# Performance work log

Hardware: AMD Instinct MI355X
Metric: run time of the kernel (lower is better)

## Reference

```python
import jax, jax.numpy as jnp
import numpy as np

N = 20000      # nodes
E1 = 100000    # topo (2d) edges
E2 = 100000    # distance edges
HID = 128      # hidden_size
N2D = 128      # node_embed_size_2d
E2D = 64       # edge_embed_size_2d
EF = 128       # edge_feat_size
ET = 32        # edge_type_size
NRBF = 64
CUT = 6.0


def rbf_expand(d):
    # Gaussian radial basis with cosine cutoff envelope, d: [E]
    centers = jnp.linspace(0.0, CUT, NRBF)
    width = CUT / NRBF
    env = 0.5 * (jnp.cos(jnp.pi * jnp.clip(d / CUT, 0.0, 1.0)) + 1.0)
    return jnp.exp(-((d[:, None] - centers) ** 2) / (2.0 * width * width)) * env[:, None]


def setup_inputs() -> dict:
    key = jax.random.key(0)
    ks = jax.random.split(key, 20)
    s = 0.02
    return {
        "H": jax.random.normal(ks[0], (N, HID), jnp.float32),
        "V": jax.random.normal(ks[1], (N, HID, 3), jnp.float32),
        "Z": jax.random.normal(ks[2], (N, 3), jnp.float32) * 3.0,
        "layer_i": 0,
        "H_2d": jax.random.normal(ks[3], (N, N2D), jnp.float32),
        "mask_2d": jnp.ones((N,), bool),
        "E2d_idx": jax.random.randint(ks[4], (2, E1), 0, N),
        "E2d_feat": jax.random.normal(ks[5], (E2D, E1), jnp.float32),
        "Z_3d": jax.random.normal(ks[6], (N, 3), jnp.float32) * 3.0,
        "mask_3d": jnp.ones((N,), bool),
        "Edist_idx": jax.random.randint(ks[7], (2, E2), 0, N),
        "Edist_val": jax.random.uniform(ks[8], (E2,), jnp.float32) * CUT,
        "virtual_node_embed": jax.random.normal(ks[9], (1, N2D), jnp.float32),
        "edge_type_embed": jax.random.normal(ks[10], (3, ET), jnp.float32),
        "W_rbf": jax.random.normal(ks[11], (EF, NRBF), jnp.float32) * s,
        "W_e2d": jax.random.normal(ks[12], (EF, E2D), jnp.float32) * s,
        "W_i": jax.random.normal(ks[13], (HID, HID + N2D), jnp.float32) * s,
        "W_phi1": jax.random.normal(ks[14], (HID, HID + EF + ET), jnp.float32) * s,
        "b_phi1": jnp.zeros((HID,), jnp.float32),
        "W_phi2": jax.random.normal(ks[15], (3 * HID, HID), jnp.float32) * s,
        "b_phi2": jnp.zeros((3 * HID,), jnp.float32),
        "W_msg": jax.random.normal(ks[16], (3 * HID, NRBF), jnp.float32) * s,
        "b_msg": jnp.zeros((3 * HID,), jnp.float32),
    }


def reference(H, V, Z, layer_i, H_2d, mask_2d, E2d_idx, E2d_feat, Z_3d, mask_3d,
              Edist_idx, Edist_val, virtual_node_embed, edge_type_embed,
              W_rbf, W_e2d, W_i, W_phi1, b_phi1, W_phi2, b_phi2, W_msg, b_msg):
    n = H.shape[0]
    # mask_3d is all-True in this fixture => n_cond_3d == n (static shapes)
    nodes_real = jnp.concatenate([H, H_2d], axis=-1)                       # [n, h1+h2]
    virt = jnp.broadcast_to(virtual_node_embed, (n, virtual_node_embed.shape[1]))
    nodes_virt = jnp.concatenate([H, virt], axis=-1)                        # [n, h1+h2]
    nodes = jnp.concatenate([nodes_real, nodes_virt], axis=0) @ W_i.T      # [2n, h1]
    v = jnp.concatenate([V, jnp.zeros_like(V)], axis=0)                     # [2n, h1, 3]
    z = jnp.concatenate([Z, Z_3d], axis=0)                                  # [2n, 3]

    row_3d = jnp.arange(n)
    col_3d = jnp.arange(n) + n
    E3d = jnp.stack([jnp.concatenate([row_3d, col_3d]),
                     jnp.concatenate([col_3d, row_3d])], axis=0)            # [2, 2n]
    edges = jnp.concatenate([E2d_idx, E3d, Edist_idx], axis=-1)             # [2, E]
    e1, e3, e2 = E2d_idx.shape[1], E3d.shape[1], Edist_idx.shape[1]
    edge_type = jnp.concatenate([jnp.zeros((e1,), jnp.int32),
                                 jnp.ones((e3,), jnp.int32),
                                 jnp.full((e2,), 2, jnp.int32)])
    et = edge_type_embed[edge_type]                                         # [E, ET]
    attr2d = E2d_feat.T @ W_e2d.T                                           # [e1, EF]
    attr3d = jnp.zeros((e3, W_e2d.shape[0]), jnp.float32)                   # [e3, EF]
    attrd = rbf_expand(Edist_val) @ W_rbf.T                                 # [e2, EF]
    edge_attr = jnp.concatenate(
        [jnp.concatenate([attr2d, attr3d, attrd], axis=0), et], axis=-1)    # [E, EF+ET]

    # AdapterLayer: PaiNN-style equivariant message passing
    row, col = edges[0], edges[1]
    rel = z[row] - z[col]                                                   # [E, 3]
    dist = jnp.sqrt(jnp.sum(rel * rel, axis=-1) + 1e-8)                     # [E]
    unit = rel / dist[:, None]
    phi_in = jnp.concatenate([nodes[col], edge_attr], axis=-1)
    phi = jax.nn.silu(phi_in @ W_phi1.T + b_phi1) @ W_phi2.T + b_phi2       # [E, 3h]
    wd = rbf_expand(dist) @ W_msg.T + b_msg                                 # [E, 3h]
    m = phi * wd
    h = nodes.shape[1]
    s_msg, v_gate, r_gate = m[:, :h], m[:, h:2 * h], m[:, 2 * h:]
    dv = v[col] * v_gate[:, :, None] + unit[:, None, :] * r_gate[:, :, None]  # [E, h, 3]
    nn2 = nodes.shape[0]
    H_add = jax.ops.segment_sum(s_msg, row, num_segments=nn2)[:n]
    V_add = jax.ops.segment_sum(dv, row, num_segments=nn2)[:n]

    # eval-mode clamp
    H_add = jnp.clip(H_add, -100.0, 100.0)
    V_add = jnp.clip(V_add, -100.0, 100.0)

    mask_dist = jnp.zeros((n,), bool).at[Edist_idx[0]].set(True).at[Edist_idx[1]].set(True)
    update_mask = mask_2d | mask_3d | mask_dist
    H_add = jnp.where(update_mask[:, None], H_add, 0.0)
    V_add = jnp.where(update_mask[:, None, None], V_add, 0.0)
    return H_add, V_add
```

## Files before the change

### kernel.cpp

```cpp
#include <hip/hip_runtime.h>
#include <hip/hip_bf16.h>

#define NN   20000
#define E1N  100000
#define E2N  100000
#define NEFF 220000
#define TILE 64
#define NBLK ((NEFF + TILE - 1) / TILE)
#define NPAD (NBLK * TILE)
#define RBF_STEP   0.09523809523809523f
#define RBF_INV2W2 56.88888888888889f

typedef short  bf16x8 __attribute__((ext_vector_type(8)));
typedef float  f32x4  __attribute__((ext_vector_type(4)));

__device__ __forceinline__ float4 ld4(const float* p) {
    return *reinterpret_cast<const float4*>(p);
}
__device__ __forceinline__ ushort f2bf(float x) {
    __hip_bfloat16 h = __float2bfloat16(x);
    return *reinterpret_cast<ushort*>(&h);
}
__device__ __forceinline__ float bf2f(ushort u) {
    return __uint_as_float(((unsigned)u) << 16);
}
__device__ __forceinline__ float env_of(float d) {
    float x = fminf(fmaxf(d * (1.0f / 6.0f), 0.0f), 1.0f);
    return 0.5f * (__cosf(3.14159265358979f * x) + 1.0f);
}
__device__ __forceinline__ float clip100(float x) {
    return fminf(fmaxf(x, -100.f), 100.f);
}

__device__ __forceinline__ int edge_row(int eid, const int* __restrict__ E2d_idx,
                                        const int* __restrict__ Edist_idx) {
    if (eid < E1N) return E2d_idx[eid];
    if (eid < E1N + NN) return eid - E1N;
    return Edist_idx[eid - E1N - NN];
}

__global__ __launch_bounds__(256) void hist_kernel(
    const int* __restrict__ E2d_idx, const int* __restrict__ Edist_idx,
    int* __restrict__ hist) {
    int g = blockIdx.x * 256 + threadIdx.x;
    if (g < NEFF) atomicAdd(&hist[edge_row(g, E2d_idx, Edist_idx)], 1);
}

__global__ __launch_bounds__(256) void scan_kernel(
    const int* __restrict__ hist, int* __restrict__ start, int* __restrict__ cursor) {
    __shared__ int wsum[4];
    const int t = threadIdx.x;
    const int base = t * 80;
    int s = 0;
    for (int j = 0; j < 80; ++j) {
        int idx = base + j;
        if (idx < NN) s += hist[idx];
    }
    const int lane = t & 63, w = t >> 6;
    int v = s;
    for (int off = 1; off < 64; off <<= 1) {
        int x = __shfl_up(v, off, 64);
        if (lane >= off) v += x;
    }
    if (lane == 63) wsum[w] = v;
    __syncthreads();
    int woff = 0;
    for (int i = 0; i < w; ++i) woff += wsum[i];
    int run = woff + v - s;
    for (int j = 0; j < 80; ++j) {
        int idx = base + j;
        if (idx < NN) {
            start[idx] = run;
            cursor[idx] = run;
            run += hist[idx];
        }
    }
    if (t == 255) start[NN] = run;
}

__global__ __launch_bounds__(256) void scatter_kernel(
    const int* __restrict__ E2d_idx, const int* __restrict__ Edist_idx,
    int* __restrict__ cursor, int* __restrict__ order) {
    int g = blockIdx.x * 256 + threadIdx.x;
    if (g < NEFF) {
        int r = edge_row(g, E2d_idx, Edist_idx);
        int pos = atomicAdd(&cursor[r], 1);
        order[pos] = g;
    }
}

__global__ __launch_bounds__(256) void meta_kernel(
    const int* __restrict__ order, const int* __restrict__ E2d_idx,
    const int* __restrict__ Edist_idx, const float* __restrict__ Edist_val,
    const float* __restrict__ Z, const float* __restrict__ Z3d,
    int4* __restrict__ metaI, float4* __restrict__ metaF,
    float4* __restrict__ metaU) {
    int g = blockIdx.x * 256 + threadIdx.x;
    if (g >= NPAD) return;
    int eid = (g < NEFF) ? order[g] : -1;
    int row, col, ty, e2 = 0; float dval = 0.f;
    if (eid < 0)             { ty = 1; row = -1; col = 0; }
    else if (eid < E1N)      { ty = 0; row = E2d_idx[eid]; col = E2d_idx[E1N + eid]; e2 = eid; }
    else if (eid < E1N + NN) { ty = 1; int jj = eid - E1N; row = jj; col = jj + NN; }
    else { ty = 2; int g2 = eid - E1N - NN;
           row = Edist_idx[g2]; col = Edist_idx[E2N + g2]; dval = Edist_val[g2]; }
    int rs = (row < 0) ? 0 : row;
    float prx = Z[rs * 3], pry = Z[rs * 3 + 1], prz = Z[rs * 3 + 2];
    float pcx, pcy, pcz;
    if (col < NN) { pcx = Z[col * 3]; pcy = Z[col * 3 + 1]; pcz = Z[col * 3 + 2]; }
    else { int c = col - NN; pcx = Z3d[c * 3]; pcy = Z3d[c * 3 + 1]; pcz = Z3d[c * 3 + 2]; }
    float dx = prx - pcx, dy = pry - pcy, dz = prz - pcz;
    float dist = sqrtf(dx * dx + dy * dy + dz * dz + 1e-8f);
    float inv = 1.0f / dist;
    int vcol = (col < NN) ? col : -1;
    metaI[g] = make_int4(col, row, ty, e2);
    metaF[g] = make_float4(dist, dval, env_of(dist), env_of(dval));
    metaU[g] = (row >= 0)
        ? make_float4(dx * inv, dy * inv, dz * inv, __int_as_float(vcol))
        : make_float4(0.f, 0.f, 0.f, __int_as_float(-1));
}

__global__ __launch_bounds__(256) void prep_kernel(
    const float* __restrict__ W_phi1, const float* __restrict__ b_phi1,
    const float* __restrict__ W_e2d, const float* __restrict__ W_rbf,
    const float* __restrict__ W_phi2, const float* __restrict__ W_msg,
    const float* __restrict__ et, const float* __restrict__ W_i,
    ushort* __restrict__ W1c, ushort* __restrict__ W2b,
    ushort* __restrict__ Wmb, float* __restrict__ b_type,
    ushort* __restrict__ Wib) {
    int g = blockIdx.x * 256 + threadIdx.x;
    if (g < 32768) {
        int n = g >> 8, k = g & 255;
        float v;
        if (k < 128) v = W_phi1[n * 288 + k];
        else {
            int kk = k - 128;
            const float* Wsel = (kk < 64) ? W_e2d : W_rbf;
            int j = kk & 63;
            float s = 0.f;
            for (int a = 0; a < 128; ++a) s += W_phi1[n * 288 + 128 + a] * Wsel[a * 64 + j];
            v = s;
        }
        W1c[n * 256 + k] = f2bf(v);
    } else if (g < 81920) {
        int q = g - 32768; W2b[q] = f2bf(W_phi2[q]);
    } else if (g < 106496) {
        int q = g - 81920; Wmb[q] = f2bf(W_msg[q]);
    } else if (g < 106880) {
        int q = g - 106496; int ty = q >> 7, n = q & 127;
        float s = b_phi1[n];
        for (int a = 0; a < 32; ++a) s += W_phi1[n * 288 + 256 + a] * et[ty * 32 + a];
        b_type[q] = s;
    } else if (g < 139648) {
        int q = g - 106880; Wib[q] = f2bf(W_i[q]);
    }
}

__global__ __launch_bounds__(256) void featT_kernel(
    const float* __restrict__ feat, ushort* __restrict__ featTb) {
    __shared__ float tile[64][65];
    const int t = threadIdx.x;
    const int cbase = blockIdx.x * 64;
    for (int i = t; i < 64 * 64; i += 256) {
        int k = i >> 6, e = i & 63;
        tile[k][e] = (cbase + e < E1N) ? feat[(size_t)k * E1N + cbase + e] : 0.f;
    }
    __syncthreads();
    for (int i = t; i < 64 * 64; i += 256) {
        int e = i >> 6, k = i & 63;
        if (cbase + e < E1N) featTb[(size_t)(cbase + e) * 64 + k] = f2bf(tile[k][e]);
    }
}

__global__ __launch_bounds__(256, 2) void nodes_mfma_kernel(
    const float* __restrict__ H, const float* __restrict__ H2d,
    const float* __restrict__ virt, const ushort* __restrict__ Wib,
    ushort* __restrict__ nodesb) {
    __shared__ ushort A[64][264];
    __shared__ ushort WB[128][132];

    const int t = threadIdx.x;
    const int gbase = blockIdx.x * 64;

    for (int i = t; i < 64 * 64; i += 256) {
        int e = i >> 6, q = i & 63;
        int row = gbase + e;
        float4 v;
        if (q < 32)          v = ld4(H + (size_t)((row < NN) ? row : row - NN) * 128 + q * 4);
        else if (row < NN)   v = ld4(H2d + (size_t)row * 128 + (q - 32) * 4);
        else                 v = ld4(virt + (q - 32) * 4);
        ushort tmp[4] = {f2bf(v.x), f2bf(v.y), f2bf(v.z), f2bf(v.w)};
        *reinterpret_cast<uint2*>(&A[e][q * 4]) = *reinterpret_cast<const uint2*>(tmp);
    }
    for (int i = t; i < 128 * 16; i += 256) {
        int n = i >> 4, q = i & 15;
        *reinterpret_cast<uint4*>(&WB[n][q * 8]) =
            *reinterpret_cast<const uint4*>(Wib + (size_t)n * 256 + q * 8);
    }
    __syncthreads();

    const int w  = t >> 6, lane = t & 63;
    const int mh = w >> 1, nh = w & 1;
    const int lr = lane >> 4, lc = lane & 15;
    const int ar0 = mh * 32 + lc;

    f32x4 acc[2][4];
#pragma unroll
    for (int mt = 0; mt < 2; ++mt)
#pragma unroll
        for (int nt = 0; nt < 4; ++nt) acc[mt][nt] = (f32x4){0.f, 0.f, 0.f, 0.f};
#pragma unroll
    for (int ks = 0; ks < 4; ++ks) {
        bf16x8 a0 = *reinterpret_cast<const bf16x8*>(&A[ar0][ks * 32 + lr * 8]);
        bf16x8 a1 = *reinterpret_cast<const bf16x8*>(&A[ar0 + 16][ks * 32 + lr * 8]);
#pragma unroll
        for (int nt = 0; nt < 4; ++nt) {
            int n = nh * 64 + nt * 16 + lc;
            bf16x8 b = *reinterpret_cast<const bf16x8*>(&WB[n][ks * 32 + lr * 8]);
            acc[0][nt] = __builtin_amdgcn_mfma_f32_16x16x32_bf16(a0, b, acc[0][nt], 0, 0, 0);
            acc[1][nt] = __builtin_amdgcn_mfma_f32_16x16x32_bf16(a1, b, acc[1][nt], 0, 0, 0);
        }
    }
    __syncthreads();
    for (int i = t; i < 128 * 16; i += 256) {
        int n = i >> 4, q = i & 15;
        *reinterpret_cast<uint4*>(&WB[n][q * 8]) =
            *reinterpret_cast<const uint4*>(Wib + (size_t)n * 256 + 128 + q * 8);
    }
    __syncthreads();
#pragma unroll
    for (int ks = 4; ks < 8; ++ks) {
        bf16x8 a0 = *reinterpret_cast<const bf16x8*>(&A[ar0][ks * 32 + lr * 8]);
        bf16x8 a1 = *reinterpret_cast<const bf16x8*>(&A[ar0 + 16][ks * 32 + lr * 8]);
#pragma unroll
        for (int nt = 0; nt < 4; ++nt) {
            int n = nh * 64 + nt * 16 + lc;
            bf16x8 b = *reinterpret_cast<const bf16x8*>(&WB[n][(ks - 4) * 32 + lr * 8]);
            acc[0][nt] = __builtin_amdgcn_mfma_f32_16x16x32_bf16(a0, b, acc[0][nt], 0, 0, 0);
            acc[1][nt] = __builtin_amdgcn_mfma_f32_16x16x32_bf16(a1, b, acc[1][nt], 0, 0, 0);
        }
    }
#pragma unroll
    for (int mt = 0; mt < 2; ++mt)
#pragma unroll
        for (int nt = 0; nt < 4; ++nt)
#pragma unroll
            for (int r = 0; r < 4; ++r) {
                int e  = mh * 32 + mt * 16 + lr * 4 + r;
                int ch = nh * 64 + nt * 16 + lc;
                nodesb[(size_t)(gbase + e) * 128 + ch] = f2bf(acc[mt][nt][r]);
            }
}

__global__ __launch_bounds__(256, 2) void edge1_kernel(
    const ushort* __restrict__ nodesb, const ushort* __restrict__ featTb,
    const ushort* __restrict__ W1c, const ushort* __restrict__ W2b,
    const ushort* __restrict__ Wmb, const float* __restrict__ b_type,
    const float* __restrict__ b_phi2, const float* __restrict__ b_msg,
    const int4* __restrict__ metaI, const float4* __restrict__ metaF,
    ushort* __restrict__ payloadM) {

    __shared__ ushort A1f[TILE * 264 + 256];
    __shared__ ushort WB[128][132];
    __shared__ float  s_bt[3][128];
    __shared__ int    s_col[TILE], s_ty[TILE], s_e2[TILE];
    __shared__ float  s_dval[TILE], s_env2[TILE];

    ushort* hidp  = A1f;
    ushort* m_lds = A1f + 8704;

    const int t = threadIdx.x;
    const int gbase = blockIdx.x * TILE;

    if (t < TILE) {
        int4 mi = metaI[gbase + t];
        s_col[t] = mi.x; s_ty[t] = mi.z; s_e2[t] = mi.w;
        float4 mf = metaF[gbase + t];
        s_dval[t] = mf.y; s_env2[t] = mf.w;
    }
    for (int i = t; i < 384; i += 256) ((float*)s_bt)[i] = b_type[i];
    __syncthreads();

    for (int i = t; i < TILE * 16; i += 256) {
        int e = i >> 4, q = i & 15;
        *reinterpret_cast<uint4*>(&A1f[e * 264 + q * 8]) =
            *reinterpret_cast<const uint4*>(nodesb + (size_t)s_col[e] * 128 + q * 8);
    }
    for (int i = t; i < TILE * 128; i += 256) {
        int e = i >> 7, k = i & 127;
        int ty = s_ty[e];
        ushort v = 0;
        if (ty == 0) { if (k < 64) v = featTb[(size_t)s_e2[e] * 64 + k]; }
        else if (ty == 2) {
            if (k >= 64) {
                float dd = s_dval[e] - (float)(k - 64) * RBF_STEP;
                v = f2bf(__expf(-dd * dd * RBF_INV2W2) * s_env2[e]);
            }
        }
        A1f[e * 264 + 128 + k] = v;
    }
    for (int i = t; i < 128 * 16; i += 256) {
        int n = i >> 4, q = i & 15;
        *reinterpret_cast<uint4*>(&WB[n][q * 8]) =
            *reinterpret_cast<const uint4*>(W1c + (size_t)n * 256 + q * 8);
    }
    __syncthreads();

    const int w  = t >> 6, lane = t & 63;
    const int mh = w >> 1, nh = w & 1;
    const int lr = lane >> 4, lc = lane & 15;
    const int ar0 = mh * 32 + lc;

    const float4 mfA = metaF[gbase + ar0];
    const float4 mfB = metaF[gbase + ar0 + 16];
    bf16x8 ra0[2], ra1[2];
#pragma unroll
    for (int ks = 0; ks < 2; ++ks)
#pragma unroll
        for (int j = 0; j < 8; ++j) {
            float cc = (float)(ks * 32 + lr * 8 + j) * RBF_STEP;
            float tA = mfA.x - cc, tB = mfB.x - cc;
            ra0[ks][j] = (short)f2bf(__expf(-tA * tA * RBF_INV2W2) * mfA.z);
            ra1[ks][j] = (short)f2bf(__expf(-tB * tB * RBF_INV2W2) * mfB.z);
        }

    f32x4 acc[2][4];
#pragma unroll
    for (int mt = 0; mt < 2; ++mt)
#pragma unroll
        for (int nt = 0; nt < 4; ++nt) acc[mt][nt] = (f32x4){0.f, 0.f, 0.f, 0.f};
#pragma unroll
    for (int ks = 0; ks < 4; ++ks) {
        bf16x8 a0 = *reinterpret_cast<const bf16x8*>(&A1f[ar0 * 264 + ks * 32 + lr * 8]);
        bf16x8 a1 = *reinterpret_cast<const bf16x8*>(&A1f[(ar0 + 16) * 264 + ks * 32 + lr * 8]);
#pragma unroll
        for (int nt = 0; nt < 4; ++nt) {
            int n = nh * 64 + nt * 16 + lc;
            bf16x8 b = *reinterpret_cast<const bf16x8*>(&WB[n][ks * 32 + lr * 8]);
            acc[0][nt] = __builtin_amdgcn_mfma_f32_16x16x32_bf16(a0, b, acc[0][nt], 0, 0, 0);
            acc[1][nt] = __builtin_amdgcn_mfma_f32_16x16x32_bf16(a1, b, acc[1][nt], 0, 0, 0);
        }
    }
    __syncthreads();
    for (int i = t; i < 128 * 16; i += 256) {
        int n = i >> 4, q = i & 15;
        *reinterpret_cast<uint4*>(&WB[n][q * 8]) =
            *reinterpret_cast<const uint4*>(W1c + (size_t)n * 256 + 128 + q * 8);
    }
    __syncthreads();
#pragma unroll
    for (int ks = 4; ks < 8; ++ks) {
        bf16x8 a0 = *reinterpret_cast<const bf16x8*>(&A1f[ar0 * 264 + ks * 32 + lr * 8]);
        bf16x8 a1 = *reinterpret_cast<const bf16x8*>(&A1f[(ar0 + 16) * 264 + ks * 32 + lr * 8]);
#pragma unroll
        for (int nt = 0; nt < 4; ++nt) {
            int n = nh * 64 + nt * 16 + lc;
            bf16x8 b = *reinterpret_cast<const bf16x8*>(&WB[n][(ks - 4) * 32 + lr * 8]);
            acc[0][nt] = __builtin_amdgcn_mfma_f32_16x16x32_bf16(a0, b, acc[0][nt], 0, 0, 0);
            acc[1][nt] = __builtin_amdgcn_mfma_f32_16x16x32_bf16(a1, b, acc[1][nt], 0, 0, 0);
        }
    }
    __syncthreads();

#pragma unroll
    for (int mt = 0; mt < 2; ++mt)
#pragma unroll
        for (int nt = 0; nt < 4; ++nt)
#pragma unroll
            for (int r = 0; r < 4; ++r) {
                int e  = mh * 32 + mt * 16 + lr * 4 + r;
                int ch = nh * 64 + nt * 16 + lc;
                float x = acc[mt][nt][r] + s_bt[s_ty[e]][ch];
                hidp[e * 136 + ch] = f2bf(x / (1.0f + __expf(-x)));
            }
    for (int i = t; i < 128 * 16; i += 256) {
        int n = i >> 4, q = i & 15;
        *reinterpret_cast<uint4*>(&WB[n][q * 8]) =
            *reinterpret_cast<const uint4*>(W2b + (size_t)n * 128 + q * 8);
    }
    __syncthreads();

    bf16x8 ha0[4], ha1[4];
#pragma unroll
    for (int ks = 0; ks < 4; ++ks) {
        ha0[ks] = *reinterpret_cast<const bf16x8*>(&hidp[ar0 * 136 + ks * 32 + lr * 8]);
        ha1[ks] = *reinterpret_cast<const bf16x8*>(&hidp[(ar0 + 16) * 136 + ks * 32 + lr * 8]);
    }

#pragma unroll
    for (int c = 0; c < 3; ++c) {
        f32x4 p[2][4], g[2][4];
#pragma unroll
        for (int mt = 0; mt < 2; ++mt)
#pragma unroll
            for (int nt = 0; nt < 4; ++nt) {
                p[mt][nt] = (f32x4){0.f, 0.f, 0.f, 0.f};
                g[mt][nt] = (f32x4){0.f, 0.f, 0.f, 0.f};
            }
#pragma unroll
        for (int ks = 0; ks < 4; ++ks) {
#pragma unroll
            for (int nt = 0; nt < 4; ++nt) {
                int n = nh * 64 + nt * 16 + lc;
                bf16x8 b = *reinterpret_cast<const bf16x8*>(&WB[n][ks * 32 + lr * 8]);
                p[0][nt] = __builtin_amdgcn_mfma_f32_16x16x32_bf16(ha0[ks], b, p[0][nt], 0, 0, 0);
                p[1][nt] = __builtin_amdgcn_mfma_f32_16x16x32_bf16(ha1[ks], b, p[1][nt], 0, 0, 0);
            }
        }
#pragma unroll
        for (int ks = 0; ks < 2; ++ks) {
#pragma unroll
            for (int nt = 0; nt < 4; ++nt) {
                int n = c * 128 + nh * 64 + nt * 16 + lc;
                bf16x8 b = *reinterpret_cast<const bf16x8*>(Wmb + (size_t)n * 64 + ks * 32 + lr * 8);
                g[0][nt] = __builtin_amdgcn_mfma_f32_16x16x32_bf16(ra0[ks], b, g[0][nt], 0, 0, 0);
                g[1][nt] = __builtin_amdgcn_mfma_f32_16x16x32_bf16(ra1[ks], b, g[1][nt], 0, 0, 0);
            }
        }
        __syncthreads();
#pragma unroll
        for (int mt = 0; mt < 2; ++mt)
#pragma unroll
            for (int nt = 0; nt < 4; ++nt) {
                int d  = nh * 64 + nt * 16 + lc;
                float b2 = b_phi2[c * 128 + d];
                float bm = b_msg[c * 128 + d];
#pragma unroll
                for (int r = 0; r < 4; ++r) {
                    int e = mh * 32 + mt * 16 + lr * 4 + r;
                    m_lds[e * 132 + d] = f2bf((p[mt][nt][r] + b2) * (g[mt][nt][r] + bm));
                }
            }
        if (c < 2) {
            for (int i = t; i < 128 * 16; i += 256) {
                int n = i >> 4, q = i & 15;
                *reinterpret_cast<uint4*>(&WB[n][q * 8]) =
                    *reinterpret_cast<const uint4*>(W2b + (size_t)((c + 1) * 128 + n) * 128 + q * 8);
            }
        }
        __syncthreads();
        for (int i = t; i < 2048; i += 256) {
            int e = i >> 5, q = i & 31;
            *reinterpret_cast<uint2*>(payloadM + (size_t)(gbase + e) * 384 + c * 128 + q * 4) =
                *reinterpret_cast<const uint2*>(m_lds + e * 132 + q * 4);
        }
    }
}

__global__ __launch_bounds__(256, 2) void edge0_kernel(
    const ushort* __restrict__ nodesb, const float* __restrict__ V,
    const float* __restrict__ Z, const float* __restrict__ Z3d,
    const int* __restrict__ E2d_idx, const float* __restrict__ E2d_feat,
    const int* __restrict__ Edist_idx, const float* __restrict__ Edist_val,
    const ushort* __restrict__ W1c, const ushort* __restrict__ W2b,
    const ushort* __restrict__ Wmb, const float* __restrict__ b_type,
    const float* __restrict__ b_phi2, const float* __restrict__ b_msg,
    float* __restrict__ Hout, float* __restrict__ Vout) {

    __shared__ ushort A1[TILE][264];
    __shared__ float  s_bt[3][128];
    __shared__ int    s_row[TILE], s_col[TILE], s_ty[TILE], s_e2[TILE], s_vcol[TILE];
    __shared__ float  s_dist[TILE], s_dval[TILE], s_env[TILE], s_env2[TILE];
    __shared__ float  s_unit[TILE][3];
    ushort (*hid)[136] = reinterpret_cast<ushort(*)[136]>(&A1[0][0]);

    const int t = threadIdx.x;
    const int gbase = blockIdx.x * TILE;
    if (t < TILE) {
        int gpos = gbase + t;
        int eid = (gpos < NEFF) ? gpos : -1;
        int row, col, ty, e2 = 0; float dval = 0.f;
        if (eid < 0)             { ty = 1; row = -1; col = 0; }
        else if (eid < E1N)      { ty = 0; row = E2d_idx[eid]; col = E2d_idx[E1N + eid]; e2 = eid; }
        else if (eid < E1N + NN) { ty = 1; int jj = eid - E1N; row = jj; col = jj + NN; }
        else { ty = 2; int g2 = eid - E1N - NN;
               row = Edist_idx[g2]; col = Edist_idx[E2N + g2]; dval = Edist_val[g2]; }
        int rs = (row < 0) ? 0 : row;
        float prx = Z[rs * 3], pry = Z[rs * 3 + 1], prz = Z[rs * 3 + 2];
        float pcx, pcy, pcz;
        if (col < NN) { pcx = Z[col * 3]; pcy = Z[col * 3 + 1]; pcz = Z[col * 3 + 2]; }
        else { int c = col - NN; pcx = Z3d[c * 3]; pcy = Z3d[c * 3 + 1]; pcz = Z3d[c * 3 + 2]; }
        float dx = prx - pcx, dy = pry - pcy, dz = prz - pcz;
        float dist = sqrtf(dx * dx + dy * dy + dz * dz + 1e-8f);
        float inv = 1.0f / dist;
        s_row[t] = row; s_col[t] = col; s_ty[t] = ty; s_e2[t] = e2;
        s_vcol[t] = (col < NN) ? col : -1;
        s_unit[t][0] = dx * inv; s_unit[t][1] = dy * inv; s_unit[t][2] = dz * inv;
        s_dist[t] = dist; s_dval[t] = dval;
        s_env[t] = env_of(dist); s_env2[t] = env_of(dval);
    }
    for (int i = t; i < 384; i += 256) ((float*)s_bt)[i] = b_type[i];
    __syncthreads();

    for (int i = t; i < TILE * 16; i += 256) {
        int e = i >> 4, q = i & 15;
        *reinterpret_cast<uint4*>(&A1[e][q * 8]) =
            *reinterpret_cast<const uint4*>(nodesb + (size_t)s_col[e] * 128 + q * 8);
    }
    for (int i = t; i < TILE * 128; i += 256) {
        int k = i >> 6, e = i & 63;
        int ty = s_ty[e];
        float v = 0.f;
        if (ty == 0) { if (k < 64) v = E2d_feat[(size_t)k * E1N + s_e2[e]]; }
        else if (ty == 2) {
            if (k >= 64) {
                float dd = s_dval[e] - (float)(k - 64) * RBF_STEP;
                v = __expf(-dd * dd * RBF_INV2W2) * s_env2[e];
            }
        }
        A1[e][128 + k] = f2bf(v);
    }
    __syncthreads();

    const int w  = t >> 6, lane = t & 63;
    const int mh = w >> 1, nh = w & 1;
    const int lr = lane >> 4, lc = lane & 15;
    const int ar0 = mh * 32 + lc;

    bf16x8 ra0[2], ra1[2];
    {
        float dA = s_dist[ar0],      eA = s_env[ar0];
        float dB = s_dist[ar0 + 16], eB = s_env[ar0 + 16];
#pragma unroll
        for (int ks = 0; ks < 2; ++ks)
#pragma unroll
            for (int j = 0; j < 8; ++j) {
                float c  = (float)(ks * 32 + lr * 8 + j) * RBF_STEP;
                float tA = dA - c, tB = dB - c;
                ra0[ks][j] = (short)f2bf(__expf(-tA * tA * RBF_INV2W2) * eA);
                ra1[ks][j] = (short)f2bf(__expf(-tB * tB * RBF_INV2W2) * eB);
            }
    }

    f32x4 acc[2][4];
#pragma unroll
    for (int mt = 0; mt < 2; ++mt)
#pragma unroll
        for (int nt = 0; nt < 4; ++nt) acc[mt][nt] = (f32x4){0.f, 0.f, 0.f, 0.f};
#pragma unroll
    for (int ks = 0; ks < 8; ++ks) {
        bf16x8 a0 = *reinterpret_cast<const bf16x8*>(&A1[ar0][ks * 32 + lr * 8]);
        bf16x8 a1 = *reinterpret_cast<const bf16x8*>(&A1[ar0 + 16][ks * 32 + lr * 8]);
#pragma unroll
        for (int nt = 0; nt < 4; ++nt) {
            int n = nh * 64 + nt * 16 + lc;
            bf16x8 b = *reinterpret_cast<const bf16x8*>(W1c + (size_t)n * 256 + ks * 32 + lr * 8);
            acc[0][nt] = __builtin_amdgcn_mfma_f32_16x16x32_bf16(a0, b, acc[0][nt], 0, 0, 0);
            acc[1][nt] = __builtin_amdgcn_mfma_f32_16x16x32_bf16(a1, b, acc[1][nt], 0, 0, 0);
        }
    }
    __syncthreads();
#pragma unroll
    for (int mt = 0; mt < 2; ++mt)
#pragma unroll
        for (int nt = 0; nt < 4; ++nt)
#pragma unroll
            for (int r = 0; r < 4; ++r) {
                int e  = mh * 32 + mt * 16 + lr * 4 + r;
                int ch = nh * 64 + nt * 16 + lc;
                float x = acc[mt][nt][r] + s_bt[s_ty[e]][ch];
                hid[e][ch] = f2bf(x / (1.0f + __expf(-x)));
            }
    __syncthreads();

    f32x4 vgr[2][4];
#pragma unroll
    for (int c = 0; c < 3; ++c) {
        f32x4 p[2][4], g[2][4];
#pragma unroll
        for (int mt = 0; mt < 2; ++mt)
#pragma unroll
            for (int nt = 0; nt < 4; ++nt) {
                p[mt][nt] = (f32x4){0.f, 0.f, 0.f, 0.f};
                g[mt][nt] = (f32x4){0.f, 0.f, 0.f, 0.f};
            }
#pragma unroll
        for (int ks = 0; ks < 4; ++ks) {
            bf16x8 a0 = *reinterpret_cast<const bf16x8*>(&hid[ar0][ks * 32 + lr * 8]);
            bf16x8 a1 = *reinterpret_cast<const bf16x8*>(&hid[ar0 + 16][ks * 32 + lr * 8]);
#pragma unroll
            for (int nt = 0; nt < 4; ++nt) {
                int n = c * 128 + nh * 64 + nt * 16 + lc;
                bf16x8 b = *reinterpret_cast<const bf16x8*>(W2b + (size_t)n * 128 + ks * 32 + lr * 8);
                p[0][nt] = __builtin_amdgcn_mfma_f32_16x16x32_bf16(a0, b, p[0][nt], 0, 0, 0);
                p[1][nt] = __builtin_amdgcn_mfma_f32_16x16x32_bf16(a1, b, p[1][nt], 0, 0, 0);
            }
        }
#pragma unroll
        for (int ks = 0; ks < 2; ++ks) {
#pragma unroll
            for (int nt = 0; nt < 4; ++nt) {
                int n = c * 128 + nh * 64 + nt * 16 + lc;
                bf16x8 b = *reinterpret_cast<const bf16x8*>(Wmb + (size_t)n * 64 + ks * 32 + lr * 8);
                g[0][nt] = __builtin_amdgcn_mfma_f32_16x16x32_bf16(ra0[ks], b, g[0][nt], 0, 0, 0);
                g[1][nt] = __builtin_amdgcn_mfma_f32_16x16x32_bf16(ra1[ks], b, g[1][nt], 0, 0, 0);
            }
        }
#pragma unroll
        for (int mt = 0; mt < 2; ++mt)
#pragma unroll
            for (int nt = 0; nt < 4; ++nt) {
                int d  = nh * 64 + nt * 16 + lc;
                float b2 = b_phi2[c * 128 + d];
                float bm = b_msg[c * 128 + d];
#pragma unroll
                for (int r = 0; r < 4; ++r) {
                    int e = mh * 32 + mt * 16 + lr * 4 + r;
                    float m = (p[mt][nt][r] + b2) * (g[mt][nt][r] + bm);
                    int row = s_row[e];
                    if (c == 0) {
                        if (row >= 0) unsafeAtomicAdd(&Hout[(size_t)row * 128 + d], m);
                    } else if (c == 1) {
                        vgr[mt][nt][r] = m;
                    } else if (row >= 0) {
                        float vgv = vgr[mt][nt][r];
                        int vc = s_vcol[e];
                        float vx = 0.f, vy = 0.f, vz = 0.f;
                        if (vc >= 0) {
                            const float* vp = V + ((size_t)vc * 128 + d) * 3;
                            vx = vp[0]; vy = vp[1]; vz = vp[2];
                        }
                        float* vo = Vout + ((size_t)row * 128 + d) * 3;
                        unsafeAtomicAdd(vo + 0, vx * vgv + s_unit[e][0] * m);
                        unsafeAtomicAdd(vo + 1, vy * vgv + s_unit[e][1] * m);
                        unsafeAtomicAdd(vo + 2, vz * vgv + s_unit[e][2] * m);
                    }
                }
            }
    }
}

__global__ __launch_bounds__(256) void reduce_kernel(
    const ushort* __restrict__ payloadM, const float4* __restrict__ metaU,
    const float* __restrict__ V, const int* __restrict__ start,
    float* __restrict__ Hout, float* __restrict__ Vout) {
    const int t = threadIdx.x;
    const int rbase = blockIdx.x * 4;
    const bool hside = (t < 128);
    const int d = hside ? t : (t - 128);
    for (int nr = 0; nr < 4; ++nr) {
        int r = rbase + nr;
        if (r >= NN) return;
        int a = start[r], b = start[r + 1];
        int n = b - a;
        if (hside) {
            const ushort* base = payloadM + (size_t)a * 384 + d;
            float a0 = 0.f, a1 = 0.f, a2 = 0.f, a3 = 0.f;
            int i = 0;
            for (; i + 4 <= n; i += 4) {
                a0 += bf2f(base[(size_t)i * 384]);
                a1 += bf2f(base[(size_t)(i + 1) * 384]);
                a2 += bf2f(base[(size_t)(i + 2) * 384]);
                a3 += bf2f(base[(size_t)(i + 3) * 384]);
            }
            for (; i < n; ++i) a0 += bf2f(base[(size_t)i * 384]);
            Hout[(size_t)r * 128 + d] = clip100((a0 + a1) + (a2 + a3));
        } else {
            const ushort* base = payloadM + (size_t)a * 384;
            const float4* ub = metaU + a;
            float ax = 0.f, ay = 0.f, az = 0.f;
            float bx = 0.f, by = 0.f, bz = 0.f;
            int i = 0;
            for (; i + 4 <= n; i += 4) {
                const ushort* pm0 = base + (size_t)i * 384;
                const ushort* pm1 = base + (size_t)(i + 1) * 384;
                const ushort* pm2 = base + (size_t)(i + 2) * 384;
                const ushort* pm3 = base + (size_t)(i + 3) * 384;
                float vg0 = bf2f(pm0[128 + d]), rg0 = bf2f(pm0[256 + d]);
                float vg1 = bf2f(pm1[128 + d]), rg1 = bf2f(pm1[256 + d]);
                float vg2 = bf2f(pm2[128 + d]), rg2 = bf2f(pm2[256 + d]);
                float vg3 = bf2f(pm3[128 + d]), rg3 = bf2f(pm3[256 + d]);
                float4 u0 = ub[i], u1 = ub[i + 1], u2 = ub[i + 2], u3 = ub[i + 3];
                int vc0 = __float_as_int(u0.w);
                int vc1 = __float_as_int(u1.w);
                int vc2 = __float_as_int(u2.w);
                int vc3 = __float_as_int(u3.w);
                if (vc0 >= 0) {
                    const float* vp = V + (size_t)vc0 * 384 + d * 3;
                    ax += vg0 * vp[0]; ay += vg0 * vp[1]; az += vg0 * vp[2];
                }
                if (vc1 >= 0) {
                    const float* vp = V + (size_t)vc1 * 384 + d * 3;
                    bx += vg1 * vp[0]; by += vg1 * vp[1]; bz += vg1 * vp[2];
                }
                if (vc2 >= 0) {
                    const float* vp = V + (size_t)vc2 * 384 + d * 3;
                    ax += vg2 * vp[0]; ay += vg2 * vp[1]; az += vg2 * vp[2];
                }
                if (vc3 >= 0) {
                    const float* vp = V + (size_t)vc3 * 384 + d * 3;
                    bx += vg3 * vp[0]; by += vg3 * vp[1]; bz += vg3 * vp[2];
                }
                ax += rg0 * u0.x; ay += rg0 * u0.y; az += rg0 * u0.z;
                bx += rg1 * u1.x; by += rg1 * u1.y; bz += rg1 * u1.z;
                ax += rg2 * u2.x; ay += rg2 * u2.y; az += rg2 * u2.z;
                bx += rg3 * u3.x; by += rg3 * u3.y; bz += rg3 * u3.z;
            }
            for (; i < n; ++i) {
                const ushort* pm0 = base + (size_t)i * 384;
                float vg0 = bf2f(pm0[128 + d]), rg0 = bf2f(pm0[256 + d]);
                float4 u0 = ub[i];
                int vc0 = __float_as_int(u0.w);
                if (vc0 >= 0) {
                    const float* vp = V + (size_t)vc0 * 384 + d * 3;
                    ax += vg0 * vp[0]; ay += vg0 * vp[1]; az += vg0 * vp[2];
                }
                ax += rg0 * u0.x; ay += rg0 * u0.y; az += rg0 * u0.z;
            }
            float* vo = Vout + (size_t)r * 384 + d * 3;
            vo[0] = clip100(ax + bx);
            vo[1] = clip100(ay + by);
            vo[2] = clip100(az + bz);
        }
    }
}

extern "C" void kernel_launch(void* const* d_in, const int* in_sizes, int n_in,
                              void* d_out, int out_size, void* d_ws, size_t ws_size,
                              hipStream_t stream) {
    const float* H         = (const float*)d_in[0];
    const float* V         = (const float*)d_in[1];
    const float* Z         = (const float*)d_in[2];
    const float* H2d       = (const float*)d_in[4];
    const int*   E2d_idx   = (const int*)d_in[6];
    const float* E2d_feat  = (const float*)d_in[7];
    const float* Z3d       = (const float*)d_in[8];
    const int*   Edist_idx = (const int*)d_in[10];
    const float* Edist_val = (const float*)d_in[11];
    const float* virt      = (const float*)d_in[12];
    const float* et        = (const float*)d_in[13];
    const float* W_rbf     = (const float*)d_in[14];
    const float* W_e2d     = (const float*)d_in[15];
    const float* W_i       = (const float*)d_in[16];
    const float* W_phi1    = (const float*)d_in[17];
    const float* b_phi1    = (const float*)d_in[18];
    const float* W_phi2    = (const float*)d_in[19];
    const float* b_phi2    = (const float*)d_in[20];
    const float* W_msg     = (const float*)d_in[21];
    const float* b_msg     = (const float*)d_in[22];

    ushort* nodesb  = (ushort*)d_ws;
    ushort* W1c     = nodesb + 5120000;
    ushort* W2b     = W1c + 32768;
    ushort* Wmb     = W2b + 49152;
    ushort* Wib     = Wmb + 24576;
    float*  b_type  = (float*)(Wib + 32768);
    ushort* featTb  = (ushort*)(b_type + 384);
    int*    hist    = (int*)(featTb + (size_t)E1N * 64);
    int*    cursor  = hist + NN;
    int*    start   = cursor + NN;
    int*    order   = start + NN + 1;
    int4*   metaI   = (int4*)(((size_t)(order + NPAD) + 15) & ~(size_t)15);
    float4* metaF   = (float4*)(metaI + NPAD);
    float4* metaU   = metaF + NPAD;

    size_t fixed = (size_t)((char*)(metaU + NPAD) - (char*)d_ws);
    size_t poff  = (fixed + 255) & ~(size_t)255;
    size_t need  = poff + (size_t)NPAD * 384 * sizeof(ushort);
    const bool big = (ws_size >= need);
    ushort* payloadM = (ushort*)((char*)d_ws + poff);

    float* Hout = (float*)d_out;
    float* Vout = Hout + (size_t)NN * 128;

    prep_kernel<<<(139648 + 255) / 256, 256, 0, stream>>>(
        W_phi1, b_phi1, W_e2d, W_rbf, W_phi2, W_msg, et, W_i,
        W1c, W2b, Wmb, b_type, Wib);
    nodes_mfma_kernel<<<(2 * NN) / 64, 256, 0, stream>>>(H, H2d, virt, Wib, nodesb);

    if (big) {
        hipMemsetAsync(hist, 0, NN * sizeof(int), stream);
        featT_kernel<<<(E1N + 63) / 64, 256, 0, stream>>>(E2d_feat, featTb);
        hist_kernel<<<(NEFF + 255) / 256, 256, 0, stream>>>(E2d_idx, Edist_idx, hist);
        scan_kernel<<<1, 256, 0, stream>>>(hist, start, cursor);
        scatter_kernel<<<(NEFF + 255) / 256, 256, 0, stream>>>(E2d_idx, Edist_idx, cursor, order);
        meta_kernel<<<(NPAD + 255) / 256, 256, 0, stream>>>(
            order, E2d_idx, Edist_idx, Edist_val, Z, Z3d, metaI, metaF, metaU);
        edge1_kernel<<<NBLK, 256, 0, stream>>>(
            nodesb, featTb, W1c, W2b, Wmb, b_type, b_phi2, b_msg,
            metaI, metaF, payloadM);
        reduce_kernel<<<(NN + 3) / 4, 256, 0, stream>>>(
            payloadM, metaU, V, start, Hout, Vout);
    } else {
        hipMemsetAsync(d_out, 0, (size_t)out_size * sizeof(float), stream);
        edge0_kernel<<<NBLK, 256, 0, stream>>>(
            nodesb, V, Z, Z3d, E2d_idx, E2d_feat, Edist_idx, Edist_val,
            W1c, W2b, Wmb, b_type, b_phi2, b_msg, Hout, Vout);
    }
}
```

Baseline: 399.5 us.

## Halve edge1 weight LDS tile to fit three blocks per CU

Stages the phi1 and phi2 weights through shared memory in 64-wide K chunks instead of 128-wide. This shrinks the hidden-activation stride, lowering per-block LDS so the launch bound can rise from two to three blocks per CU. The aim is higher occupancy to hide gather and global-load latency. In exchange it doubles the number of weight reload phases and block barriers, which are still not overlapped with the MFMA work.

```diff
diff --git a/kernel.cpp b/kernel.cpp
--- a/kernel.cpp
+++ b/kernel.cpp
@@ -252,7 +252,7 @@
             }
 }
 
-__global__ __launch_bounds__(256, 2) void edge1_kernel(
+__global__ __launch_bounds__(256, 3) void edge1_kernel(
     const ushort* __restrict__ nodesb, const ushort* __restrict__ featTb,
     const ushort* __restrict__ W1c, const ushort* __restrict__ W2b,
     const ushort* __restrict__ Wmb, const float* __restrict__ b_type,
@@ -260,14 +260,14 @@
     const int4* __restrict__ metaI, const float4* __restrict__ metaF,
     ushort* __restrict__ payloadM) {
 
-    __shared__ ushort A1f[TILE * 264 + 256];
-    __shared__ ushort WB[128][132];
+    __shared__ ushort A1f[16896];
+    __shared__ ushort WB[128 * 68];
     __shared__ float  s_bt[3][128];
     __shared__ int    s_col[TILE], s_ty[TILE], s_e2[TILE];
     __shared__ float  s_dval[TILE], s_env2[TILE];
 
     ushort* hidp  = A1f;
-    ushort* m_lds = A1f + 8704;
+    ushort* m_lds = A1f + 8448;
 
     const int t = threadIdx.x;
     const int gbase = blockIdx.x * TILE;
@@ -299,9 +299,9 @@
         }
         A1f[e * 264 + 128 + k] = v;
     }
-    for (int i = t; i < 128 * 16; i += 256) {
-        int n = i >> 4, q = i & 15;
-        *reinterpret_cast<uint4*>(&WB[n][q * 8]) =
+    for (int i = t; i < 1024; i += 256) {
+        int n = i >> 3, q = i & 7;
+        *reinterpret_cast<uint4*>(&WB[n * 68 + q * 8]) =
             *reinterpret_cast<const uint4*>(W1c + (size_t)n * 256 + q * 8);
     }
     __syncthreads();
@@ -330,37 +330,36 @@
 #pragma unroll
         for (int nt = 0; nt < 4; ++nt) acc[mt][nt] = (f32x4){0.f, 0.f, 0.f, 0.f};
 #pragma unroll
-    for (int ks = 0; ks < 4; ++ks) {
-        bf16x8 a0 = *reinterpret_cast<const bf16x8*>(&A1f[ar0 * 264 + ks * 32 + lr * 8]);
-        bf16x8 a1 = *reinterpret_cast<const bf16x8*>(&A1f[(ar0 + 16) * 264 + ks * 32 + lr * 8]);
-#pragma unroll
-        for (int nt = 0; nt < 4; ++nt) {
-            int n = nh * 64 + nt * 16 + lc;
-            bf16x8 b = *reinterpret_cast<const bf16x8*>(&WB[n][ks * 32 + lr * 8]);
-            acc[0][nt] = __builtin_amdgcn_mfma_f32_16x16x32_bf16(a0, b, acc[0][nt], 0, 0, 0);
-            acc[1][nt] = __builtin_amdgcn_mfma_f32_16x16x32_bf16(a1, b, acc[1][nt], 0, 0, 0);
-        }
-    }
-    __syncthreads();
-    for (int i = t; i < 128 * 16; i += 256) {
-        int n = i >> 4, q = i & 15;
-        *reinterpret_cast<uint4*>(&WB[n][q * 8]) =
-            *reinterpret_cast<const uint4*>(W1c + (size_t)n * 256 + 128 + q * 8);
-    }
-    __syncthreads();
-#pragma unroll
-    for (int ks = 4; ks < 8; ++ks) {
-        bf16x8 a0 = *reinterpret_cast<const bf16x8*>(&A1f[ar0 * 264 + ks * 32 + lr * 8]);
-        bf16x8 a1 = *reinterpret_cast<const bf16x8*>(&A1f[(ar0 + 16) * 264 + ks * 32 + lr * 8]);
-#pragma unroll
-        for (int nt = 0; nt < 4; ++nt) {
-            int n = nh * 64 + nt * 16 + lc;
-            bf16x8 b = *reinterpret_cast<const bf16x8*>(&WB[n][(ks - 4) * 32 + lr * 8]);
-            acc[0][nt] = __builtin_amdgcn_mfma_f32_16x16x32_bf16(a0, b, acc[0][nt], 0, 0, 0);
-            acc[1][nt] = __builtin_amdgcn_mfma_f32_16x16x32_bf16(a1, b, acc[1][nt], 0, 0, 0);
-        }
-    }
-    __syncthreads();
+    for (int s = 0; s < 4; ++s) {
+#pragma unroll
+        for (int ksl = 0; ksl < 2; ++ksl) {
+            int ks = s * 2 + ksl;
+            bf16x8 a0 = *reinterpret_cast<const bf16x8*>(&A1f[ar0 * 264 + ks * 32 + lr * 8]);
+            bf16x8 a1 = *reinterpret_cast<const bf16x8*>(&A1f[(ar0 + 16) * 264 + ks * 32 + lr * 8]);
+#pragma unroll
+            for (int nt = 0; nt < 4; ++nt) {
+                int n = nh * 64 + nt * 16 + lc;
+                bf16x8 b = *reinterpret_cast<const bf16x8*>(&WB[n * 68 + ksl * 32 + lr * 8]);
+                acc[0][nt] = __builtin_amdgcn_mfma_f32_16x16x32_bf16(a0, b, acc[0][nt], 0, 0, 0);
+                acc[1][nt] = __builtin_amdgcn_mfma_f32_16x16x32_bf16(a1, b, acc[1][nt], 0, 0, 0);
+            }
+        }
+        __syncthreads();
+        if (s < 3) {
+            for (int i = t; i < 1024; i += 256) {
+                int n = i >> 3, q = i & 7;
+                *reinterpret_cast<uint4*>(&WB[n * 68 + q * 8]) =
+                    *reinterpret_cast<const uint4*>(W1c + (size_t)n * 256 + (s + 1) * 64 + q * 8);
+            }
+        } else {
+            for (int i = t; i < 1024; i += 256) {
+                int n = i >> 3, q = i & 7;
+                *reinterpret_cast<uint4*>(&WB[n * 68 + q * 8]) =
+                    *reinterpret_cast<const uint4*>(W2b + (size_t)n * 128 + q * 8);
+            }
+        }
+        __syncthreads();
+    }
 
 #pragma unroll
     for (int mt = 0; mt < 2; ++mt)
@@ -371,20 +370,15 @@
                 int e  = mh * 32 + mt * 16 + lr * 4 + r;
                 int ch = nh * 64 + nt * 16 + lc;
                 float x = acc[mt][nt][r] + s_bt[s_ty[e]][ch];
-                hidp[e * 136 + ch] = f2bf(x / (1.0f + __expf(-x)));
-            }
-    for (int i = t; i < 128 * 16; i += 256) {
-        int n = i >> 4, q = i & 15;
-        *reinterpret_cast<uint4*>(&WB[n][q * 8]) =
-            *reinterpret_cast<const uint4*>(W2b + (size_t)n * 128 + q * 8);
-    }
+                hidp[e * 132 + ch] = f2bf(x / (1.0f + __expf(-x)));
+            }
     __syncthreads();
 
     bf16x8 ha0[4], ha1[4];
 #pragma unroll
     for (int ks = 0; ks < 4; ++ks) {
-        ha0[ks] = *reinterpret_cast<const bf16x8*>(&hidp[ar0 * 136 + ks * 32 + lr * 8]);
-        ha1[ks] = *reinterpret_cast<const bf16x8*>(&hidp[(ar0 + 16) * 136 + ks * 32 + lr * 8]);
+        ha0[ks] = *reinterpret_cast<const bf16x8*>(&hidp[ar0 * 132 + ks * 32 + lr * 8]);
+        ha1[ks] = *reinterpret_cast<const bf16x8*>(&hidp[(ar0 + 16) * 132 + ks * 32 + lr * 8]);
     }
 
 #pragma unroll
@@ -398,14 +392,30 @@
                 g[mt][nt] = (f32x4){0.f, 0.f, 0.f, 0.f};
             }
 #pragma unroll
-        for (int ks = 0; ks < 4; ++ks) {
-#pragma unroll
-            for (int nt = 0; nt < 4; ++nt) {
-                int n = nh * 64 + nt * 16 + lc;
-                bf16x8 b = *reinterpret_cast<const bf16x8*>(&WB[n][ks * 32 + lr * 8]);
-                p[0][nt] = __builtin_amdgcn_mfma_f32_16x16x32_bf16(ha0[ks], b, p[0][nt], 0, 0, 0);
-                p[1][nt] = __builtin_amdgcn_mfma_f32_16x16x32_bf16(ha1[ks], b, p[1][nt], 0, 0, 0);
-            }
+        for (int s2 = 0; s2 < 2; ++s2) {
+#pragma unroll
+            for (int ksl = 0; ksl < 2; ++ksl) {
+                int hk = s2 * 2 + ksl;
+#pragma unroll
+                for (int nt = 0; nt < 4; ++nt) {
+                    int n = nh * 64 + nt * 16 + lc;
+                    bf16x8 b = *reinterpret_cast<const bf16x8*>(&WB[n * 68 + ksl * 32 + lr * 8]);
+                    p[0][nt] = __builtin_amdgcn_mfma_f32_16x16x32_bf16(ha0[hk], b, p[0][nt], 0, 0, 0);
+                    p[1][nt] = __builtin_amdgcn_mfma_f32_16x16x32_bf16(ha1[hk], b, p[1][nt], 0, 0, 0);
+                }
+            }
+            __syncthreads();
+            int nxt = c * 2 + s2 + 1;
+            if (nxt < 6) {
+                int cn = nxt >> 1, sn = nxt & 1;
+                for (int i = t; i < 1024; i += 256) {
+                    int n = i >> 3, q = i & 7;
+                    *reinterpret_cast<uint4*>(&WB[n * 68 + q * 8]) =
+                        *reinterpret_cast<const uint4*>(
+                            W2b + (size_t)(cn * 128 + n) * 128 + sn * 64 + q * 8);
+                }
+            }
+            __syncthreads();
         }
 #pragma unroll
         for (int ks = 0; ks < 2; ++ks) {
@@ -417,7 +427,6 @@
                 g[1][nt] = __builtin_amdgcn_mfma_f32_16x16x32_bf16(ra1[ks], b, g[1][nt], 0, 0, 0);
             }
         }
-        __syncthreads();
 #pragma unroll
         for (int mt = 0; mt < 2; ++mt)
 #pragma unroll
@@ -431,13 +440,6 @@
                     m_lds[e * 132 + d] = f2bf((p[mt][nt][r] + b2) * (g[mt][nt][r] + bm));
                 }
             }
-        if (c < 2) {
-            for (int i = t; i < 128 * 16; i += 256) {
-                int n = i >> 4, q = i & 15;
-                *reinterpret_cast<uint4*>(&WB[n][q * 8]) =
-                    *reinterpret_cast<const uint4*>(W2b + (size_t)((c + 1) * 128 + n) * 128 + q * 8);
-            }
-        }
         __syncthreads();
         for (int i = t; i < 2048; i += 256) {
             int e = i >> 5, q = i & 31;
```

Result: slower. 442.0 us (+10.6%).
